# Performance work log

Hardware: AMD Instinct MI355X
Metric: run time of the kernel (lower is better)

Reference implementation:

```python
import jax, jax.numpy as jnp
import numpy as np

VGG_MEAN = jnp.array([0.485, 0.456, 0.406, 0.5, 0.5, 0.5], dtype=jnp.float32)
VGG_STD = jnp.array([0.229, 0.224, 0.225, 0.1, 0.1, 0.1], dtype=jnp.float32)
KSIZE = 3
STRIDE = 3


def _conv2d(x, w, b, pad):
    y = jax.lax.conv_general_dilated(
        x, w, window_strides=(1, 1), padding=[(pad, pad), (pad, pad)],
        dimension_numbers=("NCHW", "OIHW", "NCHW"))
    return y + b[None, :, None, None]


def _sub_mean(x):
    # MeanShift(1, vgg_mean, vgg_std): (x - mean) / std
    return (x - VGG_MEAN[None, :, None, None]) / VGG_STD[None, :, None, None]


def _feature_extract(x, w1, b1, w2, b2, w3, b3, w4, b4):
    x = jax.nn.relu(_conv2d(x, w1, b1, 1))
    x = jax.nn.relu(_conv2d(x, w2, b2, 1))
    x = jax.nn.relu(_conv2d(x, w3, b3, 1))
    x = _conv2d(x, w4, b4, 0)          # 1x1 conv 128->16 (BasicBlock 'map')
    return jax.nn.leaky_relu(x, 0.2)


def _unfold_k3s3(x):
    # extract_image_patches ksize=3 stride=3 'same'; H,W divisible by 3 -> no pad.
    # Returns [B, C*9, L] with torch.unfold ordering (c, kh, kw) x (row-major L).
    B, C, H, W = x.shape
    Hq, Wq = H // STRIDE, W // STRIDE
    x = x.reshape(B, C, Hq, KSIZE, Wq, KSIZE).transpose(0, 1, 3, 5, 2, 4)
    return x.reshape(B, C * KSIZE * KSIZE, Hq * Wq)


def _l2norm(x, axis):
    n = jnp.sqrt(jnp.sum(x * x, axis=axis, keepdims=True))
    return x / jnp.maximum(n, 1e-12)


def setup_inputs() -> dict:
    key = jax.random.key(0)
    ks = jax.random.split(key, 8)
    B, H, W = 2, 288, 288

    def mkw(k, shape, fan_in):
        return jax.random.normal(k, shape, jnp.float32) * (1.0 / np.sqrt(fan_in))

    return {
        "query": jax.random.normal(ks[0], (B, 6, H, W), jnp.float32),
        "key": jax.random.normal(ks[1], (B, 6, H, W), jnp.float32),
        "flag_8k": 1,
        "w1": mkw(ks[2], (64, 6, 3, 3), 6 * 9),   "b1": jnp.zeros((64,), jnp.float32),
        "w2": mkw(ks[3], (64, 64, 3, 3), 64 * 9), "b2": jnp.zeros((64,), jnp.float32),
        "w3": mkw(ks[4], (128, 64, 3, 3), 64 * 9),"b3": jnp.zeros((128,), jnp.float32),
        "w4": mkw(ks[5], (16, 128, 1, 1), 128),   "b4": jnp.zeros((16,), jnp.float32),
    }


def reference(query, key, flag_8k, w1, b1, w2, b2, w3, b3, w4, b4):
    # flag_8k=1 (static) -> skip bicubic interpolate; scale=1 -> avgpool identity
    q = _sub_mean(query)
    qf = _feature_extract(q, w1, b1, w2, b2, w3, b3, w4, b4)   # [B,16,H,W]
    B, _, H, W = qf.shape

    k = _sub_mean(key)
    kf = _feature_extract(k, w1, b1, w2, b2, w3, b3, w4, b4)   # shared encoder

    qp = _l2norm(_unfold_k3s3(qf), axis=1)                 # [B, 144, M]
    kp = _l2norm(_unfold_k3s3(kf).transpose(0, 2, 1), axis=2)  # [B, L, 144]

    y = jnp.einsum("bld,bdm->blm", kp, qp)                 # [B, L_key, M_query]
    relevance = jnp.max(y, axis=1)                         # [B, M]
    hard_indices = jnp.argmax(y, axis=1)                   # [B, M]
    relevance = relevance.reshape(B, 1, H // STRIDE, W // STRIDE)
    return relevance, hard_indices
```

## Files before the change

kernel.cpp:

```cpp
#include <hip/hip_runtime.h>

#define HH 288
#define WW 288
#define HW (HH*WW)

using f16x8  = __attribute__((ext_vector_type(8))) _Float16;
using f32x4  = __attribute__((ext_vector_type(4))) float;

__device__ __forceinline__ void fma4x8(float acc[4][8], const float4 a, const float4 b0, const float4 b1) {
  float av[4] = {a.x,a.y,a.z,a.w};
  float bv[8] = {b0.x,b0.y,b0.z,b0.w,b1.x,b1.y,b1.z,b1.w};
#pragma unroll
  for (int i=0;i<4;i++)
#pragma unroll
    for (int j=0;j<8;j++)
      acc[i][j] = fmaf(av[i], bv[j], acc[i][j]);
}

__device__ __forceinline__ void fma8x8(float acc[8][8], const float4 a0, const float4 a1,
                                       const float4 b0, const float4 b1) {
  float av[8] = {a0.x,a0.y,a0.z,a0.w,a1.x,a1.y,a1.z,a1.w};
  float bv[8] = {b0.x,b0.y,b0.z,b0.w,b1.x,b1.y,b1.z,b1.w};
#pragma unroll
  for (int i=0;i<8;i++)
#pragma unroll
    for (int j=0;j<8;j++)
      acc[i][j] = fmaf(av[i], bv[j], acc[i][j]);
}

__global__ __launch_bounds__(256) void prep_kernel(const float* __restrict__ w2, const float* __restrict__ w3,
                                                   float* __restrict__ W2t, float* __restrict__ W3t) {
  int tid = blockIdx.x*256 + threadIdx.x;
  int stride = gridDim.x*256;
  for (int e = tid; e < 9*64*64; e += stride) {
    int tap = e / 4096, ci = (e >> 6) & 63, co = e & 63;
    W2t[e] = w2[(co*64 + ci)*9 + tap];
  }
  for (int e = tid; e < 9*64*128; e += stride) {
    int tap = e / 8192, ci = (e >> 7) & 63, co = e & 127;
    W3t[e] = w3[(co*64 + ci)*9 + tap];
  }
}

__global__ __launch_bounds__(256) void conv1_kernel(const float* __restrict__ q, const float* __restrict__ k,
                                                    const float* __restrict__ w1, const float* __restrict__ b1,
                                                    float* __restrict__ X1) {
  __shared__ float Bs[54*128];
  __shared__ float As[54*64];
  __shared__ float bias_s[64];
  int img = blockIdx.z;
  const float* src = (img < 2) ? (q + (size_t)img*6*HW) : (k + (size_t)(img-2)*6*HW);
  int y0 = blockIdx.y*4, x0 = blockIdx.x*32;
  int tid = threadIdx.x;
  for (int e = tid; e < 54*64; e += 256) {
    int kk = e >> 6, co = e & 63;
    int ci = kk/9, tap = kk%9;
    As[e] = w1[(co*6 + ci)*9 + tap];
  }
  if (tid < 64) bias_s[tid] = b1[tid];
  const float mean[6] = {0.485f,0.456f,0.406f,0.5f,0.5f,0.5f};
  const float istd[6] = {1.0f/0.229f,1.0f/0.224f,1.0f/0.225f,10.0f,10.0f,10.0f};
  for (int e = tid; e < 54*128; e += 256) {
    int kk = e >> 7, p = e & 127;
    int ci = kk/9, tap = kk%9;
    int dy = tap/3, dx = tap%3, r = p>>5, xx = p&31;
    int gy = y0 + r + dy - 1, gx = x0 + xx + dx - 1;
    float v = 0.f;
    if (gy >= 0 && gy < HH && gx >= 0 && gx < WW)
      v = (src[(ci*HH + gy)*WW + gx] - mean[ci]) * istd[ci];
    Bs[e] = v;
  }
  __syncthreads();
  int tp = tid & 15, tc = tid >> 4;
  float acc[4][8] = {};
#pragma unroll 6
  for (int kk = 0; kk < 54; kk++) {
    float4 a  = *(float4*)&As[kk*64 + tc*4];
    float4 v0 = *(float4*)&Bs[kk*128 + tp*4];
    float4 v1 = *(float4*)&Bs[kk*128 + 64 + tp*4];
    fma4x8(acc, a, v0, v1);
  }
  int rA = tp>>3, cb = (tp&7)*4;
#pragma unroll
  for (int i=0;i<4;i++){
    int co = tc*4 + i;
    float b = bias_s[co];
    float o[8];
#pragma unroll
    for (int j=0;j<8;j++) o[j] = fmaxf(acc[i][j] + b, 0.f);
    size_t rowb = ((size_t)(img*64+co)*HH);
    *(float4*)&X1[(rowb + y0 + rA)*WW + x0 + cb]     = make_float4(o[0],o[1],o[2],o[3]);
    *(float4*)&X1[(rowb + y0 + 2 + rA)*WW + x0 + cb] = make_float4(o[4],o[5],o[6],o[7]);
  }
}

__global__ __launch_bounds__(256) void conv2_kernel(const float* __restrict__ X1, const float* __restrict__ W2t,
                                                    const float* __restrict__ b2, float* __restrict__ X2) {
  __shared__ float Bs[36*256];
  __shared__ float As[36*64];
  __shared__ float bias_s[64];
  int img = blockIdx.z, y0 = blockIdx.y*8, x0 = blockIdx.x*32;
  int tid = threadIdx.x;
  if (tid < 64) bias_s[tid] = b2[tid];
  const float* src = X1 + (size_t)img*64*HW;
  int aoff[9];
#pragma unroll
  for (int j=0;j<9;j++){
    int e = tid + j*256;
    int kk = e >> 6, co = e & 63;
    int ci = kk/9, tap = kk%9;
    aoff[j] = (tap*64 + ci)*64 + co;
  }
  int boff[36];
#pragma unroll
  for (int j=0;j<36;j++){
    int e = tid + j*256;
    int kk = e >> 8, p = e & 255;
    int ci = kk/9, tap = kk%9;
    int dy = tap/3, dx = tap%3, r = p>>5, xx = p&31;
    int gy = y0 + r + dy - 1, gx = x0 + xx + dx - 1;
    bool ok = (gy >= 0 && gy < HH && gx >= 0 && gx < WW);
    boff[j] = ok ? (ci*HW + gy*WW + gx) : -1;
  }
  float aPre[9], bPre[36];
#pragma unroll
  for (int j=0;j<9;j++) aPre[j] = W2t[aoff[j]];
#pragma unroll
  for (int j=0;j<36;j++){ int o = boff[j]; bPre[j] = (o >= 0) ? src[o] : 0.f; }
  int tp = tid & 15, tc = tid >> 4;
  float acc[4][16] = {};
  for (int c0 = 0; c0 < 64; c0 += 4) {
    __syncthreads();
#pragma unroll
    for (int j=0;j<9;j++)  As[tid + j*256] = aPre[j];
#pragma unroll
    for (int j=0;j<36;j++) Bs[tid + j*256] = bPre[j];
    __syncthreads();
    if (c0 < 60) {
#pragma unroll
      for (int j=0;j<9;j++)  aPre[j] = W2t[aoff[j] + (c0+4)*64];
#pragma unroll
      for (int j=0;j<36;j++){ int o = boff[j]; bPre[j] = (o >= 0) ? src[(size_t)(c0+4)*HW + o] : 0.f; }
    }
#pragma unroll 4
    for (int kk = 0; kk < 36; kk++) {
      float4 a  = *(float4*)&As[kk*64 + tc*4];
      float4 v0 = *(float4*)&Bs[kk*256 + tp*4];
      float4 v1 = *(float4*)&Bs[kk*256 + 64 + tp*4];
      float4 v2 = *(float4*)&Bs[kk*256 + 128 + tp*4];
      float4 v3 = *(float4*)&Bs[kk*256 + 192 + tp*4];
      float av[4] = {a.x,a.y,a.z,a.w};
      float bv[16] = {v0.x,v0.y,v0.z,v0.w, v1.x,v1.y,v1.z,v1.w,
                      v2.x,v2.y,v2.z,v2.w, v3.x,v3.y,v3.z,v3.w};
#pragma unroll
      for (int i=0;i<4;i++)
#pragma unroll
        for (int jj=0;jj<16;jj++)
          acc[i][jj] = fmaf(av[i], bv[jj], acc[i][jj]);
    }
  }
#pragma unroll
  for (int i=0;i<4;i++){
    int co = tc*4 + i;
    float b = bias_s[co];
    size_t rowb = ((size_t)(img*64+co)*HH);
#pragma unroll
    for (int j4=0;j4<4;j4++){
      int p = j4*64 + tp*4;
      int r = p>>5, xx = p&31;
      float4 o4 = make_float4(fmaxf(acc[i][j4*4+0] + b, 0.f),
                              fmaxf(acc[i][j4*4+1] + b, 0.f),
                              fmaxf(acc[i][j4*4+2] + b, 0.f),
                              fmaxf(acc[i][j4*4+3] + b, 0.f));
      *(float4*)&X2[(rowb + y0 + r)*WW + x0 + xx] = o4;
    }
  }
}

__global__ __launch_bounds__(256) void conv3_kernel(const float* __restrict__ X2, const float* __restrict__ W3t,
                                                    const float* __restrict__ b3, const float* __restrict__ w4,
                                                    const float* __restrict__ b4, float* __restrict__ F) {
  __shared__ float smem[9216];
  __shared__ float b3s[128];
  __shared__ float b4s[16];
  float* Bs = smem;
  float* As = smem + 4608;
  int img = blockIdx.z, y0 = blockIdx.y*4, x0 = blockIdx.x*32;
  int tid = threadIdx.x;
  if (tid < 128) b3s[tid] = b3[tid];
  if (tid < 16)  b4s[tid] = b4[tid];
  const float* src = X2 + (size_t)img*64*HW;
  int aoff[18];
#pragma unroll
  for (int j=0;j<18;j++){
    int e = tid + j*256;
    int kk = e >> 7, co = e & 127;
    int ci = kk/9, tap = kk%9;
    aoff[j] = (tap*64 + ci)*128 + co;
  }
  int boff[18];
#pragma unroll
  for (int j=0;j<18;j++){
    int e = tid + j*256;
    int kk = e >> 7, p = e & 127;
    int ci = kk/9, tap = kk%9;
    int dy = tap/3, dx = tap%3, r = p>>5, xx = p&31;
    int gy = y0 + r + dy - 1, gx = x0 + xx + dx - 1;
    bool ok = (gy >= 0 && gy < HH && gx < WW && gx >= 0);
    boff[j] = ok ? (ci*HW + gy*WW + gx) : -1;
  }
  float aPre[18], bPre[18];
#pragma unroll
  for (int j=0;j<18;j++) aPre[j] = W3t[aoff[j]];
#pragma unroll
  for (int j=0;j<18;j++){ int o = boff[j]; bPre[j] = (o >= 0) ? src[o] : 0.f; }
  int tp = tid & 15, tc = tid >> 4;
  float acc[8][8] = {};
  for (int c0 = 0; c0 < 64; c0 += 4) {
    __syncthreads();
#pragma unroll
    for (int j=0;j<18;j++) As[tid + j*256] = aPre[j];
#pragma unroll
    for (int j=0;j<18;j++) Bs[tid + j*256] = bPre[j];
    __syncthreads();
    if (c0 < 60) {
#pragma unroll
      for (int j=0;j<18;j++) aPre[j] = W3t[aoff[j] + (c0+4)*128];
#pragma unroll
      for (int j=0;j<18;j++){ int o = boff[j]; bPre[j] = (o >= 0) ? src[(size_t)(c0+4)*HW + o] : 0.f; }
    }
#pragma unroll 4
    for (int kk = 0; kk < 36; kk++) {
      float4 a0 = *(float4*)&As[kk*128 + tc*4];
      float4 a1 = *(float4*)&As[kk*128 + 64 + tc*4];
      float4 v0 = *(float4*)&Bs[kk*128 + tp*4];
      float4 v1 = *(float4*)&Bs[kk*128 + 64 + tp*4];
      fma8x8(acc, a0, a1, v0, v1);
    }
  }
#pragma unroll
  for (int i=0;i<8;i++){
    int co = (i<4) ? (tc*4+i) : (64 + tc*4 + i - 4);
    float b = b3s[co];
#pragma unroll
    for (int j=0;j<8;j++) acc[i][j] = fmaxf(acc[i][j] + b, 0.f);
  }
  __syncthreads();
  float* w4s = smem;
  float* red = smem + 2048;
  for (int e = tid; e < 2048; e += 256) w4s[e] = w4[e];
  __syncthreads();
  for (int op = 0; op < 8; op++) {
    float pout[2][8];
#pragma unroll
    for (int oo=0;oo<2;oo++){
      const float* wr = &w4s[(op*2+oo)*128];
      float wv[8];
#pragma unroll
      for (int i=0;i<8;i++) wv[i] = wr[(i<4) ? (tc*4+i) : (64 + tc*4 + i - 4)];
#pragma unroll
      for (int j=0;j<8;j++){
        float s = 0.f;
#pragma unroll
        for (int i=0;i<8;i++) s = fmaf(wv[i], acc[i][j], s);
        pout[oo][j] = s;
      }
    }
    if (op) __syncthreads();
#pragma unroll
    for (int oo=0;oo<2;oo++)
#pragma unroll
      for (int j=0;j<8;j++){
        int px = (j<4) ? (tp*4+j) : (64 + tp*4 + j - 4);
        red[(oo*128 + px)*17 + tc] = pout[oo][j];
      }
    __syncthreads();
    {
      int oo = tid >> 7, p = tid & 127;
      float s = 0.f;
#pragma unroll
      for (int t=0;t<16;t++) s += red[(oo*128+p)*17 + t];
      int o = op*2 + oo;
      s += b4s[o];
      s = (s >= 0.f) ? s : 0.2f*s;
      int pr = p >> 5, px = p & 31;
      F[((size_t)(img*16 + o)*HH + y0+pr)*WW + x0+px] = s;
    }
  }
}

__global__ __launch_bounds__(256) void unfold_norm_kernel(const float* __restrict__ F, float* __restrict__ P,
                                                          float* __restrict__ Kt,
                                                          _Float16* __restrict__ Ph, _Float16* __restrict__ Pl) {
  __shared__ float tile[16*3*288];
  __shared__ float invn[96];
  int qy = blockIdx.x, img = blockIdx.y, tid = threadIdx.x;
  const float* src = F + (size_t)img*16*HW;
  for (int e = tid; e < 16*3*288; e += 256) {
    int c = e/864, rem = e%864;
    int kh = rem/288, xx = rem%288;
    tile[e] = src[((size_t)c*HH + qy*3+kh)*WW + xx];
  }
  __syncthreads();
  if (tid < 96) {
    float s = 0.f;
    for (int c=0;c<16;c++)
#pragma unroll
      for (int kh=0;kh<3;kh++)
#pragma unroll
        for (int kw=0;kw<3;kw++){
          float v = tile[(c*3+kh)*288 + tid*3+kw];
          s = fmaf(v, v, s);
        }
    invn[tid] = 1.f / fmaxf(sqrtf(s), 1e-12f);
  }
  __syncthreads();
  for (int e = tid; e < 96*160; e += 256) {
    int qx = e/160, d = e%160;
    float v = 0.f;
    if (d < 144) {
      int c = d/9, rem = d%9, kh = rem/3, kw = rem%3;
      v = tile[(c*3+kh)*288 + qx*3+kw] * invn[qx];
    }
    _Float16 hi;
    if (__builtin_fabsf(v) < 6.1035156e-5f) hi = (_Float16)0.f;
    else hi = (_Float16)v;
    float r = v - (float)hi;
    _Float16 lo = (_Float16)(r * 4096.f);
    size_t base = ((size_t)img*9216 + qy*96 + qx)*160 + d;
    Ph[base] = hi;
    Pl[base] = lo;
  }
  if (img < 2) {
    for (int e = tid; e < 96*144; e += 256) {
      int qx = e/144, d = e%144;
      int c = d/9, rem = d%9, kh = rem/3, kw = rem%3;
      P[((size_t)img*9216 + qy*96+qx)*144 + d] = tile[(c*3+kh)*288 + qx*3+kw] * invn[qx];
    }
  } else {
    for (int e = tid; e < 96*144; e += 256) {
      int d = e/96, qx = e%96;
      int c = d/9, rem = d%9, kh = rem/3, kw = rem%3;
      Kt[((size_t)(img-2)*144 + d)*9216 + qy*96 + qx] = tile[(c*3+kh)*288 + qx*3+kw] * invn[qx];
    }
  }
}

__global__ __launch_bounds__(256) void passA_kernel(const _Float16* __restrict__ Ph,
                                                    const _Float16* __restrict__ Pl,
                                                    float* __restrict__ TM) {
  int qg = blockIdx.x, part = blockIdx.y, b = blockIdx.z;
  int tid = threadIdx.x;
  int w = tid >> 6, lane = tid & 63;
  int quad = lane >> 4, lm = lane & 15;
  int m0 = qg*128 + w*32;
  const _Float16* Phq = Ph + (size_t)b*9216*160;
  const _Float16* Plq = Pl + (size_t)b*9216*160;
  const _Float16* Phk = Ph + (size_t)(2+b)*9216*160;
  const _Float16* Plk = Pl + (size_t)(2+b)*9216*160;
  f16x8 qh[2][5], ql[2][5];
#pragma unroll
  for (int ms=0; ms<2; ms++)
#pragma unroll
    for (int kc=0; kc<5; kc++){
      size_t off = (size_t)(m0 + ms*16 + lm)*160 + kc*32 + quad*8;
      qh[ms][kc] = *(const f16x8*)(Phq + off);
      ql[ms][kc] = *(const f16x8*)(Plq + off);
    }
  for (int t = 0; t < 12; t++) {
    int lt = part*12 + t;
    int l0 = lt*128;
    float rmax[2] = {-3e38f, -3e38f};
#pragma unroll
    for (int ls=0; ls<8; ls++){
      size_t rowoff = (size_t)(l0 + ls*16 + lm)*160 + quad*8;
      f32x4 accA[2] = {{0.f,0.f,0.f,0.f},{0.f,0.f,0.f,0.f}};
      f32x4 accB[2] = {{0.f,0.f,0.f,0.f},{0.f,0.f,0.f,0.f}};
#pragma unroll
      for (int kc=0; kc<5; kc++){
        f16x8 ahv = *(const f16x8*)(Phk + rowoff + kc*32);
        f16x8 alv = *(const f16x8*)(Plk + rowoff + kc*32);
#pragma unroll
        for (int ms=0; ms<2; ms++){
          accA[ms] = __builtin_amdgcn_mfma_f32_16x16x32_f16(ahv, qh[ms][kc], accA[ms], 0, 0, 0);
          accB[ms] = __builtin_amdgcn_mfma_f32_16x16x32_f16(ahv, ql[ms][kc], accB[ms], 0, 0, 0);
          accB[ms] = __builtin_amdgcn_mfma_f32_16x16x32_f16(alv, qh[ms][kc], accB[ms], 0, 0, 0);
        }
      }
#pragma unroll
      for (int ms=0; ms<2; ms++){
        float m01 = fmaxf(accA[ms][0] + accB[ms][0]*2.44140625e-4f,
                          accA[ms][1] + accB[ms][1]*2.44140625e-4f);
        float m23 = fmaxf(accA[ms][2] + accB[ms][2]*2.44140625e-4f,
                          accA[ms][3] + accB[ms][3]*2.44140625e-4f);
        rmax[ms] = fmaxf(rmax[ms], fmaxf(m01, m23));
      }
    }
#pragma unroll
    for (int ms=0; ms<2; ms++){
      float v = rmax[ms];
      v = fmaxf(v, __shfl_xor(v, 16, 64));
      v = fmaxf(v, __shfl_xor(v, 32, 64));
      if (quad == 0) TM[((size_t)(b*9216 + m0 + ms*16 + lm))*72 + lt] = v;
    }
  }
}

__global__ __launch_bounds__(128) void passB_kernel(const float* __restrict__ P,
                                                    const float* __restrict__ Kt,
                                                    const float* __restrict__ TM,
                                                    float* __restrict__ out) {
  __shared__ float qrow[144];
  __shared__ float tmx[72];
  __shared__ float rv[128];
  __shared__ int   ri[128];
  int m = blockIdx.x, b = blockIdx.y, tid = threadIdx.x;
  const float* Q = P + ((size_t)(b*9216) + m)*144;
  const float* Kb = Kt + (size_t)b*144*9216;
  if (tid < 36) *(float4*)&qrow[tid*4] = *(const float4*)&Q[tid*4];
  if (tid < 72) tmx[tid] = TM[((size_t)(b*9216 + m))*72 + tid];
  __syncthreads();
  float M = -3e38f;
#pragma unroll 8
  for (int t = 0; t < 72; t++) M = fmaxf(M, tmx[t]);
  float T = M - 1e-4f;
  float bv = -3e38f; int bi = 0;
  for (int lt = 0; lt < 72; lt++) {
    if (tmx[lt] < T) continue;
    int l = lt*128 + tid;
    float s = 0.f;
#pragma unroll 16
    for (int d = 0; d < 144; d++)
      s = fmaf(Kb[(size_t)d*9216 + l], qrow[d], s);
    if (s > bv) { bv = s; bi = l; }
  }
  rv[tid] = bv; ri[tid] = bi;
  __syncthreads();
  for (int off = 64; off > 0; off >>= 1) {
    if (tid < off) {
      float v2 = rv[tid+off]; int i2 = ri[tid+off];
      if (v2 > rv[tid] || (v2 == rv[tid] && i2 < ri[tid])) { rv[tid] = v2; ri[tid] = i2; }
    }
    __syncthreads();
  }
  if (tid == 0) {
    out[(size_t)b*9216 + m] = rv[0];
    out[2*9216 + (size_t)b*9216 + m] = (float)ri[0];
  }
}

extern "C" void kernel_launch(void* const* d_in, const int* in_sizes, int n_in,
                              void* d_out, int out_size, void* d_ws, size_t ws_size,
                              hipStream_t stream) {
  (void)in_sizes; (void)n_in; (void)out_size; (void)ws_size;
  const float* query = (const float*)d_in[0];
  const float* key   = (const float*)d_in[1];
  const float* w1 = (const float*)d_in[3];
  const float* b1 = (const float*)d_in[4];
  const float* w2 = (const float*)d_in[5];
  const float* b2 = (const float*)d_in[6];
  const float* w3 = (const float*)d_in[7];
  const float* b3 = (const float*)d_in[8];
  const float* w4 = (const float*)d_in[9];
  const float* b4 = (const float*)d_in[10];

  float* ws = (float*)d_ws;
  size_t oX1  = 0;
  size_t oX2  = oX1 + (size_t)4*64*HW;
  size_t oF   = oX2 + (size_t)4*64*HW;
  size_t oP   = oF  + (size_t)4*16*HW;
  size_t oW2t = oP  + (size_t)2*9216*144;
  size_t oW3t = oW2t + (size_t)9*64*64;
  float* X1  = ws + oX1;
  float* X2  = ws + oX2;
  float* F   = ws + oF;
  float* P   = ws + oP;
  float* W2t = ws + oW2t;
  float* W3t = ws + oW3t;
  _Float16* Ph = (_Float16*)(ws + oX1);
  _Float16* Pl = (_Float16*)(ws + oX1 + 3*1024*1024);
  float*    Kt = ws + oX1 + 6*1024*1024;
  float*    TM = ws + oX1 + 9*1024*1024;

  hipLaunchKernelGGL(prep_kernel,        dim3(64),      dim3(256), 0, stream, w2, w3, W2t, W3t);
  hipLaunchKernelGGL(conv1_kernel,       dim3(9,72,4),  dim3(256), 0, stream, query, key, w1, b1, X1);
  hipLaunchKernelGGL(conv2_kernel,       dim3(9,36,4),  dim3(256), 0, stream, X1, W2t, b2, X2);
  hipLaunchKernelGGL(conv3_kernel,       dim3(9,72,4),  dim3(256), 0, stream, X2, W3t, b3, w4, b4, F);
  hipLaunchKernelGGL(unfold_norm_kernel, dim3(96,4),    dim3(256), 0, stream, F, P, Kt, Ph, Pl);
  hipLaunchKernelGGL(passA_kernel,       dim3(72,6,2),  dim3(256), 0, stream, Ph, Pl, TM);
  hipLaunchKernelGGL(passB_kernel,       dim3(9216,2),  dim3(128), 0, stream, P, Kt, TM, (float*)d_out);
}
```

Before: 1.743 ms.

## Double conv3 pixel tile to 8 rows and transpose TM layout

The conv3 kernel now covers an 8x32 pixel tile per block instead of 4x32. Each thread accumulates an 8x16 register tile, so every loaded weight is reused across twice as many pixels, and the grid along y is halved. The cost is more registers (128 accumulators plus 36 prefetch values) and 54KB of LDS, which may lower occupancy. Separately, the TM max table is stored as [b][lt][m] rather than [b][m][lt], which changes the write and read coalescing between passA and passB.

```diff
diff --git a/kernel.cpp b/kernel.cpp
--- a/kernel.cpp
+++ b/kernel.cpp
@@ -12,17 +12,6 @@
   float bv[8] = {b0.x,b0.y,b0.z,b0.w,b1.x,b1.y,b1.z,b1.w};
 #pragma unroll
   for (int i=0;i<4;i++)
-#pragma unroll
-    for (int j=0;j<8;j++)
-      acc[i][j] = fmaf(av[i], bv[j], acc[i][j]);
-}
-
-__device__ __forceinline__ void fma8x8(float acc[8][8], const float4 a0, const float4 a1,
-                                       const float4 b0, const float4 b1) {
-  float av[8] = {a0.x,a0.y,a0.z,a0.w,a1.x,a1.y,a1.z,a1.w};
-  float bv[8] = {b0.x,b0.y,b0.z,b0.w,b1.x,b1.y,b1.z,b1.w};
-#pragma unroll
-  for (int i=0;i<8;i++)
 #pragma unroll
     for (int j=0;j<8;j++)
       acc[i][j] = fmaf(av[i], bv[j], acc[i][j]);
@@ -180,12 +169,12 @@
 __global__ __launch_bounds__(256) void conv3_kernel(const float* __restrict__ X2, const float* __restrict__ W3t,
                                                     const float* __restrict__ b3, const float* __restrict__ w4,
                                                     const float* __restrict__ b4, float* __restrict__ F) {
-  __shared__ float smem[9216];
+  __shared__ float smem[13824];
   __shared__ float b3s[128];
   __shared__ float b4s[16];
   float* Bs = smem;
-  float* As = smem + 4608;
-  int img = blockIdx.z, y0 = blockIdx.y*4, x0 = blockIdx.x*32;
+  float* As = smem + 9216;
+  int img = blockIdx.z, y0 = blockIdx.y*8, x0 = blockIdx.x*32;
   int tid = threadIdx.x;
   if (tid < 128) b3s[tid] = b3[tid];
   if (tid < 16)  b4s[tid] = b4[tid];
@@ -198,44 +187,53 @@
     int ci = kk/9, tap = kk%9;
     aoff[j] = (tap*64 + ci)*128 + co;
   }
-  int boff[18];
-#pragma unroll
-  for (int j=0;j<18;j++){
+  int boff[36];
+#pragma unroll
+  for (int j=0;j<36;j++){
     int e = tid + j*256;
-    int kk = e >> 7, p = e & 127;
+    int kk = e >> 8, p = e & 255;
     int ci = kk/9, tap = kk%9;
     int dy = tap/3, dx = tap%3, r = p>>5, xx = p&31;
     int gy = y0 + r + dy - 1, gx = x0 + xx + dx - 1;
-    bool ok = (gy >= 0 && gy < HH && gx < WW && gx >= 0);
+    bool ok = (gy >= 0 && gy < HH && gx >= 0 && gx < WW);
     boff[j] = ok ? (ci*HW + gy*WW + gx) : -1;
   }
-  float aPre[18], bPre[18];
+  float aPre[18], bPre[36];
 #pragma unroll
   for (int j=0;j<18;j++) aPre[j] = W3t[aoff[j]];
 #pragma unroll
-  for (int j=0;j<18;j++){ int o = boff[j]; bPre[j] = (o >= 0) ? src[o] : 0.f; }
+  for (int j=0;j<36;j++){ int o = boff[j]; bPre[j] = (o >= 0) ? src[o] : 0.f; }
   int tp = tid & 15, tc = tid >> 4;
-  float acc[8][8] = {};
+  float acc[8][16] = {};
   for (int c0 = 0; c0 < 64; c0 += 4) {
     __syncthreads();
 #pragma unroll
     for (int j=0;j<18;j++) As[tid + j*256] = aPre[j];
 #pragma unroll
-    for (int j=0;j<18;j++) Bs[tid + j*256] = bPre[j];
+    for (int j=0;j<36;j++) Bs[tid + j*256] = bPre[j];
     __syncthreads();
     if (c0 < 60) {
 #pragma unroll
       for (int j=0;j<18;j++) aPre[j] = W3t[aoff[j] + (c0+4)*128];
 #pragma unroll
-      for (int j=0;j<18;j++){ int o = boff[j]; bPre[j] = (o >= 0) ? src[(size_t)(c0+4)*HW + o] : 0.f; }
-    }
-#pragma unroll 4
+      for (int j=0;j<36;j++){ int o = boff[j]; bPre[j] = (o >= 0) ? src[(size_t)(c0+4)*HW + o] : 0.f; }
+    }
+#pragma unroll 2
     for (int kk = 0; kk < 36; kk++) {
       float4 a0 = *(float4*)&As[kk*128 + tc*4];
       float4 a1 = *(float4*)&As[kk*128 + 64 + tc*4];
-      float4 v0 = *(float4*)&Bs[kk*128 + tp*4];
-      float4 v1 = *(float4*)&Bs[kk*128 + 64 + tp*4];
-      fma8x8(acc, a0, a1, v0, v1);
+      float4 v0 = *(float4*)&Bs[kk*256 + tp*4];
+      float4 v1 = *(float4*)&Bs[kk*256 + 64 + tp*4];
+      float4 v2 = *(float4*)&Bs[kk*256 + 128 + tp*4];
+      float4 v3 = *(float4*)&Bs[kk*256 + 192 + tp*4];
+      float av[8] = {a0.x,a0.y,a0.z,a0.w, a1.x,a1.y,a1.z,a1.w};
+      float bv[16] = {v0.x,v0.y,v0.z,v0.w, v1.x,v1.y,v1.z,v1.w,
+                      v2.x,v2.y,v2.z,v2.w, v3.x,v3.y,v3.z,v3.w};
+#pragma unroll
+      for (int i=0;i<8;i++)
+#pragma unroll
+        for (int jj=0;jj<16;jj++)
+          acc[i][jj] = fmaf(av[i], bv[jj], acc[i][jj]);
     }
   }
 #pragma unroll
@@ -243,7 +241,7 @@
     int co = (i<4) ? (tc*4+i) : (64 + tc*4 + i - 4);
     float b = b3s[co];
 #pragma unroll
-    for (int j=0;j<8;j++) acc[i][j] = fmaxf(acc[i][j] + b, 0.f);
+    for (int jj=0;jj<16;jj++) acc[i][jj] = fmaxf(acc[i][jj] + b, 0.f);
   }
   __syncthreads();
   float* w4s = smem;
@@ -251,7 +249,7 @@
   for (int e = tid; e < 2048; e += 256) w4s[e] = w4[e];
   __syncthreads();
   for (int op = 0; op < 8; op++) {
-    float pout[2][8];
+    float pout[2][16];
 #pragma unroll
     for (int oo=0;oo<2;oo++){
       const float* wr = &w4s[(op*2+oo)*128];
@@ -259,27 +257,27 @@
 #pragma unroll
       for (int i=0;i<8;i++) wv[i] = wr[(i<4) ? (tc*4+i) : (64 + tc*4 + i - 4)];
 #pragma unroll
-      for (int j=0;j<8;j++){
+      for (int jj=0;jj<16;jj++){
         float s = 0.f;
 #pragma unroll
-        for (int i=0;i<8;i++) s = fmaf(wv[i], acc[i][j], s);
-        pout[oo][j] = s;
+        for (int i=0;i<8;i++) s = fmaf(wv[i], acc[i][jj], s);
+        pout[oo][jj] = s;
       }
     }
     if (op) __syncthreads();
 #pragma unroll
     for (int oo=0;oo<2;oo++)
 #pragma unroll
-      for (int j=0;j<8;j++){
-        int px = (j<4) ? (tp*4+j) : (64 + tp*4 + j - 4);
-        red[(oo*128 + px)*17 + tc] = pout[oo][j];
+      for (int jj=0;jj<16;jj++){
+        int p = (jj>>2)*64 + tp*4 + (jj&3);
+        red[(oo*256 + p)*17 + tc] = pout[oo][jj];
       }
     __syncthreads();
-    {
-      int oo = tid >> 7, p = tid & 127;
+    for (int e = tid; e < 512; e += 256) {
+      int oo = e >> 8, p = e & 255;
       float s = 0.f;
 #pragma unroll
-      for (int t=0;t<16;t++) s += red[(oo*128+p)*17 + t];
+      for (int t=0;t<16;t++) s += red[(oo*256+p)*17 + t];
       int o = op*2 + oo;
       s += b4s[o];
       s = (s >= 0.f) ? s : 0.2f*s;
@@ -401,7 +399,7 @@
       float v = rmax[ms];
       v = fmaxf(v, __shfl_xor(v, 16, 64));
       v = fmaxf(v, __shfl_xor(v, 32, 64));
-      if (quad == 0) TM[((size_t)(b*9216 + m0 + ms*16 + lm))*72 + lt] = v;
+      if (quad == 0) TM[((size_t)(b*72 + lt))*9216 + m0 + ms*16 + lm] = v;
     }
   }
 }
@@ -418,7 +416,7 @@
   const float* Q = P + ((size_t)(b*9216) + m)*144;
   const float* Kb = Kt + (size_t)b*144*9216;
   if (tid < 36) *(float4*)&qrow[tid*4] = *(const float4*)&Q[tid*4];
-  if (tid < 72) tmx[tid] = TM[((size_t)(b*9216 + m))*72 + tid];
+  if (tid < 72) tmx[tid] = TM[((size_t)(b*72 + tid))*9216 + m];
   __syncthreads();
   float M = -3e38f;
 #pragma unroll 8
@@ -485,7 +483,7 @@
   hipLaunchKernelGGL(prep_kernel,        dim3(64),      dim3(256), 0, stream, w2, w3, W2t, W3t);
   hipLaunchKernelGGL(conv1_kernel,       dim3(9,72,4),  dim3(256), 0, stream, query, key, w1, b1, X1);
   hipLaunchKernelGGL(conv2_kernel,       dim3(9,36,4),  dim3(256), 0, stream, X1, W2t, b2, X2);
-  hipLaunchKernelGGL(conv3_kernel,       dim3(9,72,4),  dim3(256), 0, stream, X2, W3t, b3, w4, b4, F);
+  hipLaunchKernelGGL(conv3_kernel,       dim3(9,36,4),  dim3(256), 0, stream, X2, W3t, b3, w4, b4, F);
   hipLaunchKernelGGL(unfold_norm_kernel, dim3(96,4),    dim3(256), 0, stream, F, P, Kt, Ph, Pl);
   hipLaunchKernelGGL(passA_kernel,       dim3(72,6,2),  dim3(256), 0, stream, Ph, Pl, TM);
   hipLaunchKernelGGL(passB_kernel,       dim3(9216,2),  dim3(128), 0, stream, P, Kt, TM, (float*)d_out);
```

New measurement: 1.916 ms. +9.9%, slower.
